# Optimization experiments

Measured on AMD Instinct MI355X. Metric: run time of the kernel, lower is better.

The kernel has to match this reference:

```python
import jax, jax.numpy as jnp
import numpy as np

INPUT_DIM = 32
HIDDEN = 64
BATCH = 4096
SEQ = 256


def _uniform(key, shape, bound):
    return jax.random.uniform(key, shape, dtype=jnp.float32, minval=-bound, maxval=bound)


def setup_inputs() -> dict:
    key = jax.random.key(0)
    ks = jax.random.split(key, 16)
    kb = 1.0 / np.sqrt(HIDDEN)  # torch LSTM/Linear init bound
    x = jax.random.normal(ks[0], (BATCH, SEQ, INPUT_DIM), dtype=jnp.float32)
    # LSTM layer 0 (input_dim -> hidden), gate order i,f,g,o stacked on dim 0
    Wih0 = _uniform(ks[1], (4 * HIDDEN, INPUT_DIM), kb)
    Whh0 = _uniform(ks[2], (4 * HIDDEN, HIDDEN), kb)
    bih0 = _uniform(ks[3], (4 * HIDDEN,), kb)
    bhh0 = _uniform(ks[4], (4 * HIDDEN,), kb)
    # LSTM layer 1 (hidden -> hidden)
    Wih1 = _uniform(ks[5], (4 * HIDDEN, HIDDEN), kb)
    Whh1 = _uniform(ks[6], (4 * HIDDEN, HIDDEN), kb)
    bih1 = _uniform(ks[7], (4 * HIDDEN,), kb)
    bhh1 = _uniform(ks[8], (4 * HIDDEN,), kb)
    # MLP head
    W1 = _uniform(ks[9], (HIDDEN, HIDDEN), kb)
    b1 = _uniform(ks[10], (HIDDEN,), kb)
    W2 = _uniform(ks[11], (1, HIDDEN), kb)
    b2 = _uniform(ks[12], (1,), kb)
    return {"x": x, "Wih0": Wih0, "Whh0": Whh0, "bih0": bih0, "bhh0": bhh0,
            "Wih1": Wih1, "Whh1": Whh1, "bih1": bih1, "bhh1": bhh1,
            "W1": W1, "b1": b1, "W2": W2, "b2": b2}


def lstm_layer(x, Wih, Whh, bih, bhh):
    """x: [B,T,D] -> hidden sequence [B,T,H]. PyTorch gate order i,f,g,o."""
    B = x.shape[0]
    H = Whh.shape[1]
    # precompute input contribution for all timesteps: [B,T,4H]
    gx = jnp.einsum('btd,gd->btg', x, Wih) + bih + bhh

    def step(carry, g_t):
        h, c = carry
        g = g_t + h @ Whh.T  # [B,4H]
        i, f, gg, o = jnp.split(g, 4, axis=-1)
        i = jax.nn.sigmoid(i)
        f = jax.nn.sigmoid(f)
        gg = jnp.tanh(gg)
        o = jax.nn.sigmoid(o)
        c = f * c + i * gg
        h = o * jnp.tanh(c)
        return (h, c), h

    h0 = jnp.zeros((B, H), x.dtype)
    c0 = jnp.zeros((B, H), x.dtype)
    _, hs = jax.lax.scan(step, (h0, c0), jnp.swapaxes(gx, 0, 1))  # hs: [T,B,H]
    return jnp.swapaxes(hs, 0, 1)


def reference(x, Wih0, Whh0, bih0, bhh0, Wih1, Whh1, bih1, bhh1, W1, b1, W2, b2):
    h1 = lstm_layer(x, Wih0, Whh0, bih0, bhh0)    # [B,T,H]
    h2 = lstm_layer(h1, Wih1, Whh1, bih1, bhh1)   # [B,T,H]
    last = h2[:, -1, :]                            # [B,H]
    f = jax.nn.relu(last @ W1.T + b1)              # dropout = identity (eval)
    out = f @ W2.T + b2                            # [B,1]
    return out
```

## Files before the change

### kernel.cpp

```cpp
#include <hip/hip_runtime.h>
#include <cstdint>

typedef __attribute__((ext_vector_type(8))) _Float16 f16x8;
typedef __attribute__((ext_vector_type(4))) float f32x4;

#define SEQL 256

#define WS_B0H   0
#define WS_B0L   49152
#define WS_B1H   98304
#define WS_BIAS0 229376
#define WS_BIAS1 230400

#define ASTR 656
#define L_A  0
#define L_HD 10496
#define HDSTR 272
#define LDS_TOTAL 14848

#define NEG_L   -1.4426950408889634f
#define NEG_2L  -2.8853900817779268f
#define LO_SCALE 2048.0f
#define LO_INV   4.8828125e-4f

__device__ __forceinline__ float ex2(float x) { return __builtin_amdgcn_exp2f(x); }
__device__ __forceinline__ float rcp_(float x) { return __builtin_amdgcn_rcpf(x); }
__device__ __forceinline__ f32x4 mfma16(f16x8 a, f16x8 b, f32x4 c) {
  return __builtin_amdgcn_mfma_f32_16x16x32_f16(a, b, c, 0, 0, 0);
}
__device__ __forceinline__ f16x8 zero8() {
  f16x8 z;
#pragma unroll
  for (int i = 0; i < 8; ++i) z[i] = (_Float16)0.f;
  return z;
}

__global__ __launch_bounds__(256) void prep(
    const float* __restrict__ Wih0, const float* __restrict__ Whh0,
    const float* __restrict__ bih0, const float* __restrict__ bhh0,
    const float* __restrict__ Wih1, const float* __restrict__ Whh1,
    const float* __restrict__ bih1, const float* __restrict__ bhh1,
    unsigned char* __restrict__ ws) {
  int e = blockIdx.x * 256 + threadIdx.x;
  if (e < 24576) {
    int j = e & 7, lane = (e >> 3) & 63, nt = (e >> 9) & 15, ks = e >> 13;
    int kdim = ks * 32 + (lane >> 4) * 8 + j;
    int col = nt * 16 + (lane & 15);
    int ko = col >> 2, g = col & 3;
    float w = (kdim < 32) ? Wih0[(g * 64 + ko) * 32 + kdim]
                          : Whh0[(g * 64 + ko) * 64 + (kdim - 32)];
    w *= (g == 2) ? NEG_2L : NEG_L;
    _Float16 hi = (_Float16)w;
    _Float16 lo = (_Float16)((w - (float)hi) * LO_SCALE);
    ((_Float16*)(ws + WS_B0H))[e] = hi;
    ((_Float16*)(ws + WS_B0L))[e] = lo;
  } else if (e < 57344) {
    int r = e - 24576;
    int j = r & 7, lane = (r >> 3) & 63, nt = (r >> 9) & 15, ks = r >> 13;
    int kdim = ks * 32 + (lane >> 4) * 8 + j;
    int col = nt * 16 + (lane & 15);
    int ko = col >> 2, g = col & 3;
    float w = (kdim < 64) ? Wih1[(g * 64 + ko) * 64 + kdim]
                          : Whh1[(g * 64 + ko) * 64 + (kdim - 64)];
    w *= (g == 2) ? NEG_2L : NEG_L;
    _Float16 hi = (_Float16)w;
    _Float16 lo = (_Float16)((w - (float)hi) * LO_SCALE);
    ((_Float16*)(ws + WS_B1H))[r] = hi;
    ((_Float16*)(ws + WS_B1H + 65536))[r] = lo;
  } else if (e < 57856) {
    int r = e - 57344;
    int col = r & 255, ko = col >> 2, g = col & 3;
    float v = (r < 256) ? bih0[g * 64 + ko] + bhh0[g * 64 + ko]
                        : bih1[g * 64 + ko] + bhh1[g * 64 + ko];
    v *= (g == 2) ? NEG_2L : NEG_L;
    ((float*)(ws + (r < 256 ? WS_BIAS0 : WS_BIAS1)))[col] = v;
  }
}

__global__ __launch_bounds__(1024, 4) void lstm_mfma8(
    const float* __restrict__ x, const unsigned char* __restrict__ ws,
    const float* __restrict__ W1, const float* __restrict__ b1,
    const float* __restrict__ W2, const float* __restrict__ b2,
    float* __restrict__ out) {
  __shared__ __align__(16) unsigned char lds[LDS_TOTAL];
  const int tid = threadIdx.x;
  const int lane = tid & 63, wave = tid >> 6;
  const int q = lane >> 4, mcol = lane & 15;
  const bool grpA = wave < 8;

  f16x8 b0h[3], b0l[3], b1h[4], b1l[4];
#pragma unroll
  for (int ks = 0; ks < 3; ++ks) {
    int rec = (ks * 16 + wave) * 64 + lane;
    b0h[ks] = ((const f16x8*)(ws + WS_B0H))[rec];
    b0l[ks] = ((const f16x8*)(ws + WS_B0L))[rec];
  }
#pragma unroll
  for (int ks = 0; ks < 4; ++ks) {
    int rec = (ks * 16 + wave) * 64 + lane;
    b1h[ks] = ((const f16x8*)(ws + WS_B1H))[rec];
    b1l[ks] = ((const f16x8*)(ws + WS_B1H + 65536))[rec];
  }
  const f32x4 bias0v = ((const f32x4*)(ws + WS_BIAS0))[wave * 4 + q];
  const f32x4 bias1v = ((const f32x4*)(ws + WS_BIAS1))[wave * 4 + q];
  f32x4 z4;
  z4[0] = z4[1] = z4[2] = z4[3] = 0.f;

  for (int i = tid; i < 2624; i += 1024) ((unsigned*)(lds + L_A))[i] = 0u;

  const bool do_x = tid < 512;
  const int bx = tid >> 5, d = tid & 31;
  const float* xcol = x + (size_t)(blockIdx.x * 16 + (do_x ? bx : 0)) * (SEQL * 32) + d;
  if (do_x) {
    *(_Float16*)(lds + L_A + bx * ASTR + d * 2) = (_Float16)xcol[0];
  }

  const int ard = mcol * ASTR + q * 16;
  const int hwr = mcol * ASTR + (wave * 4 + q) * 2;

  float c1 = 0.f, c2 = 0.f, h2f = 0.f;
  f16x8 ah1[2], ah2[2], ax;
  ah1[0] = ah1[1] = ah2[0] = ah2[1] = zero8();
  __syncthreads();
  ax = *(const f16x8*)(lds + L_A + ard + 0);

  auto cell = [&](const f32x4& aH, const f32x4& aL, float& c) -> float {
    float p0 = fmaf(aL[0], LO_INV, aH[0]);
    float p1 = fmaf(aL[1], LO_INV, aH[1]);
    float p2 = fmaf(aL[2], LO_INV, aH[2]);
    float p3 = fmaf(aL[3], LO_INV, aH[3]);
    float gi = rcp_(1.f + ex2(p0));
    float gf = rcp_(1.f + ex2(p1));
    float gg = fmaf(2.f, rcp_(1.f + ex2(p2)), -1.f);
    float go = rcp_(1.f + ex2(p3));
    c = fmaf(gf, c, gi * gg);
    float tc = fmaf(2.f, rcp_(1.f + ex2(c * NEG_2L)), -1.f);
    return go * tc;
  };

  auto iter = [&](int t, int par, bool doL2) {
    const int h1s = 128 + par * 128;
    const int h2s = 384 + par * 128;
    const int xwr = (par ^ 1) * 64;
    int tn = t + 1; if (tn > SEQL - 1) tn = SEQL - 1;
    float xnext = do_x ? xcol[tn * 32] : 0.f;

    f32x4 aH0, aL0, aH1, aL1;
    auto mG0 = [&] {
      __builtin_amdgcn_s_setprio(1);
      aH0 = mfma16(b0h[0], ax, bias0v);
      aL0 = mfma16(b0l[0], ax, z4);
      aH0 = mfma16(b0h[1], ah1[0], aH0);
      aL0 = mfma16(b0l[1], ah1[0], aL0);
      aH0 = mfma16(b0h[2], ah1[1], aH0);
      aL0 = mfma16(b0l[2], ah1[1], aL0);
      __builtin_amdgcn_s_setprio(0);
    };
    auto cG0 = [&] {
      float h1 = cell(aH0, aL0, c1);
      *(_Float16*)(lds + L_A + hwr + h1s) = (_Float16)h1;
    };
    auto mG1 = [&] {
      __builtin_amdgcn_s_setprio(1);
      aH1 = mfma16(b1h[0], ah1[0], bias1v);
      aL1 = mfma16(b1l[0], ah1[0], z4);
      aH1 = mfma16(b1h[1], ah1[1], aH1);
      aL1 = mfma16(b1l[1], ah1[1], aL1);
      aH1 = mfma16(b1h[2], ah2[0], aH1);
      aL1 = mfma16(b1l[2], ah2[0], aL1);
      aH1 = mfma16(b1h[3], ah2[1], aH1);
      aL1 = mfma16(b1l[3], ah2[1], aL1);
      __builtin_amdgcn_s_setprio(0);
    };
    auto cG1 = [&] {
      if (doL2) {
        float h2 = cell(aH1, aL1, c2);
        *(_Float16*)(lds + L_A + hwr + h2s) = (_Float16)h2;
      }
    };

    if (grpA) { mG0(); cG0(); mG1(); cG1(); }
    else      { mG1(); cG1(); mG0(); cG0(); }

    if (do_x) {
      *(_Float16*)(lds + L_A + bx * ASTR + xwr + d * 2) = (_Float16)xnext;
    }
    __syncthreads();
    ax     = *(const f16x8*)(lds + L_A + ard + xwr);
    ah1[0] = *(const f16x8*)(lds + L_A + ard + h1s);
    ah1[1] = *(const f16x8*)(lds + L_A + ard + h1s + 64);
    ah2[0] = *(const f16x8*)(lds + L_A + ard + h2s);
    ah2[1] = *(const f16x8*)(lds + L_A + ard + h2s + 64);
  };

  iter(0, 0, false);
#pragma unroll 1
  for (int tp = 0; tp < 127; ++tp) {
    iter(2 * tp + 1, 1, true);
    iter(2 * tp + 2, 0, true);
  }
  iter(255, 1, true);

  {
    f32x4 aH = mfma16(b1h[0], ah1[0], bias1v);
    f32x4 aL = mfma16(b1l[0], ah1[0], z4);
    aH = mfma16(b1h[1], ah1[1], aH);
    aL = mfma16(b1l[1], ah1[1], aL);
#pragma unroll
    for (int ks = 0; ks < 2; ++ks) {
      aH = mfma16(b1h[ks + 2], ah2[ks], aH);
      aL = mfma16(b1l[ks + 2], ah2[ks], aL);
    }
    h2f = cell(aH, aL, c2);
  }

  __syncthreads();
  *(float*)(lds + L_HD + mcol * HDSTR + (wave * 4 + q) * 4) = h2f;
  __syncthreads();
  if (tid < 256) {
    const int s = tid & 15, bo = tid >> 4;
    const float* h2row = (const float*)(lds + L_HD + bo * HDSTR);
    float partial = 0.f;
#pragma unroll
    for (int kk4 = 0; kk4 < 4; ++kk4) {
      int kk = s * 4 + kk4;
      float f = b1[kk];
#pragma unroll
      for (int j = 0; j < 64; j += 4) {
        f32x4 w = *(const f32x4*)(W1 + kk * 64 + j);
        f = fmaf(w[0], h2row[j], f);
        f = fmaf(w[1], h2row[j + 1], f);
        f = fmaf(w[2], h2row[j + 2], f);
        f = fmaf(w[3], h2row[j + 3], f);
      }
      f = fmaxf(f, 0.f);
      partial = fmaf(f, W2[kk], partial);
    }
    partial += __shfl_xor(partial, 8, 64);
    partial += __shfl_xor(partial, 4, 64);
    partial += __shfl_xor(partial, 2, 64);
    partial += __shfl_xor(partial, 1, 64);
    if (s == 0) out[blockIdx.x * 16 + bo] = partial + b2[0];
  }
}

extern "C" void kernel_launch(void* const* d_in, const int* in_sizes, int n_in,
                              void* d_out, int out_size, void* d_ws, size_t ws_size,
                              hipStream_t stream) {
  const float* x    = (const float*)d_in[0];
  const float* Wih0 = (const float*)d_in[1];
  const float* Whh0 = (const float*)d_in[2];
  const float* bih0 = (const float*)d_in[3];
  const float* bhh0 = (const float*)d_in[4];
  const float* Wih1 = (const float*)d_in[5];
  const float* Whh1 = (const float*)d_in[6];
  const float* bih1 = (const float*)d_in[7];
  const float* bhh1 = (const float*)d_in[8];
  const float* W1   = (const float*)d_in[9];
  const float* b1   = (const float*)d_in[10];
  const float* W2   = (const float*)d_in[11];
  const float* b2   = (const float*)d_in[12];
  unsigned char* ws = (unsigned char*)d_ws;
  float* out = (float*)d_out;

  prep<<<(57856 + 255) / 256, 256, 0, stream>>>(Wih0, Whh0, bih0, bhh0,
                                                Wih1, Whh1, bih1, bhh1, ws);
  lstm_mfma8<<<256, 1024, 0, stream>>>(x, ws, W1, b1, W2, b2, out);
}
```

Measured before the change: 494.5 us.

## Load x directly into MFMA registers, pack h writes, and merge gate activations

Each lane now loads its x fragment straight from global memory into registers, prefetched two steps ahead and converted to fp16. This removes the LDS staging of x and shrinks the LDS tile. The h outputs are paired across lanes with a shuffle so that half the lanes write 32-bit words, and the weights' hidden dimension is permuted to match. The cell math merges reciprocals (i*g and o*tanh(c) each use one rcp). The per-wave grouped MFMA ordering and setprio are replaced by a single interleaved MFMA sequence. The x fragment is now loaded redundantly by every wave, and the new reciprocal form needs a clamp to avoid overflow.

```diff
diff --git a/kernel.cpp b/kernel.cpp
--- a/kernel.cpp
+++ b/kernel.cpp
@@ -12,11 +12,10 @@
 #define WS_BIAS0 229376
 #define WS_BIAS1 230400
 
-#define ASTR 656
-#define L_A  0
-#define L_HD 10496
+#define ASTR 528
+#define L_HD 8448
 #define HDSTR 272
-#define LDS_TOTAL 14848
+#define LDS_TOTAL 12800
 
 #define NEG_L   -1.4426950408889634f
 #define NEG_2L  -2.8853900817779268f
@@ -33,6 +32,24 @@
 #pragma unroll
   for (int i = 0; i < 8; ++i) z[i] = (_Float16)0.f;
   return z;
+}
+__device__ __forceinline__ f16x8 cvt8(f32x4 a, f32x4 b) {
+  f16x8 r;
+#pragma unroll
+  for (int j = 0; j < 4; ++j) r[j] = (_Float16)a[j];
+#pragma unroll
+  for (int j = 0; j < 4; ++j) r[4 + j] = (_Float16)b[j];
+  return r;
+}
+__device__ __forceinline__ unsigned f16bits(float h) {
+  _Float16 hf = (_Float16)h;
+  unsigned short us;
+  __builtin_memcpy(&us, &hf, 2);
+  return (unsigned)us;
+}
+
+__device__ __forceinline__ int cp(int p) {
+  return (p & ~3) | ((p & 1) << 1) | ((p >> 1) & 1);
 }
 
 __global__ __launch_bounds__(256) void prep(
@@ -48,7 +65,7 @@
     int col = nt * 16 + (lane & 15);
     int ko = col >> 2, g = col & 3;
     float w = (kdim < 32) ? Wih0[(g * 64 + ko) * 32 + kdim]
-                          : Whh0[(g * 64 + ko) * 64 + (kdim - 32)];
+                          : Whh0[(g * 64 + ko) * 64 + cp(kdim - 32)];
     w *= (g == 2) ? NEG_2L : NEG_L;
     _Float16 hi = (_Float16)w;
     _Float16 lo = (_Float16)((w - (float)hi) * LO_SCALE);
@@ -60,8 +77,8 @@
     int kdim = ks * 32 + (lane >> 4) * 8 + j;
     int col = nt * 16 + (lane & 15);
     int ko = col >> 2, g = col & 3;
-    float w = (kdim < 64) ? Wih1[(g * 64 + ko) * 64 + kdim]
-                          : Whh1[(g * 64 + ko) * 64 + (kdim - 64)];
+    float w = (kdim < 64) ? Wih1[(g * 64 + ko) * 64 + cp(kdim)]
+                          : Whh1[(g * 64 + ko) * 64 + cp(kdim - 64)];
     w *= (g == 2) ? NEG_2L : NEG_L;
     _Float16 hi = (_Float16)w;
     _Float16 lo = (_Float16)((w - (float)hi) * LO_SCALE);
@@ -77,7 +94,7 @@
   }
 }
 
-__global__ __launch_bounds__(1024, 4) void lstm_mfma8(
+__global__ __launch_bounds__(1024, 4) void lstm_mfma12(
     const float* __restrict__ x, const unsigned char* __restrict__ ws,
     const float* __restrict__ W1, const float* __restrict__ b1,
     const float* __restrict__ W2, const float* __restrict__ b2,
@@ -86,7 +103,6 @@
   const int tid = threadIdx.x;
   const int lane = tid & 63, wave = tid >> 6;
   const int q = lane >> 4, mcol = lane & 15;
-  const bool grpA = wave < 8;
 
   f16x8 b0h[3], b0l[3], b1h[4], b1l[4];
 #pragma unroll
@@ -106,91 +122,77 @@
   f32x4 z4;
   z4[0] = z4[1] = z4[2] = z4[3] = 0.f;
 
-  for (int i = tid; i < 2624; i += 1024) ((unsigned*)(lds + L_A))[i] = 0u;
-
-  const bool do_x = tid < 512;
-  const int bx = tid >> 5, d = tid & 31;
-  const float* xcol = x + (size_t)(blockIdx.x * 16 + (do_x ? bx : 0)) * (SEQL * 32) + d;
-  if (do_x) {
-    *(_Float16*)(lds + L_A + bx * ASTR + d * 2) = (_Float16)xcol[0];
-  }
+  for (int i = tid; i < 2112; i += 1024) ((unsigned*)lds)[i] = 0u;
+
+  const float* xp = x + (size_t)(blockIdx.x * 16 + mcol) * (SEQL * 32) + q * 8;
+  f16x8 ax = cvt8(*(const f32x4*)(xp), *(const f32x4*)(xp + 4));
+  f32x4 xa = *(const f32x4*)(xp + 32);
 
   const int ard = mcol * ASTR + q * 16;
-  const int hwr = mcol * ASTR + (wave * 4 + q) * 2;
 
   float c1 = 0.f, c2 = 0.f, h2f = 0.f;
-  f16x8 ah1[2], ah2[2], ax;
+  f16x8 ah1[2], ah2[2];
   ah1[0] = ah1[1] = ah2[0] = ah2[1] = zero8();
   __syncthreads();
-  ax = *(const f16x8*)(lds + L_A + ard + 0);
 
   auto cell = [&](const f32x4& aH, const f32x4& aL, float& c) -> float {
     float p0 = fmaf(aL[0], LO_INV, aH[0]);
     float p1 = fmaf(aL[1], LO_INV, aH[1]);
     float p2 = fmaf(aL[2], LO_INV, aH[2]);
     float p3 = fmaf(aL[3], LO_INV, aH[3]);
-    float gi = rcp_(1.f + ex2(p0));
-    float gf = rcp_(1.f + ex2(p1));
-    float gg = fmaf(2.f, rcp_(1.f + ex2(p2)), -1.f);
-    float go = rcp_(1.f + ex2(p3));
-    c = fmaf(gf, c, gi * gg);
-    float tc = fmaf(2.f, rcp_(1.f + ex2(c * NEG_2L)), -1.f);
-    return go * tc;
+    float A = ex2(p0), F = ex2(p1), B = ex2(p2), C = ex2(p3);
+    float ig = (1.f - B) * rcp_((1.f + A) * (1.f + B));
+    float gf = rcp_(1.f + F);
+    c = fmaf(gf, c, ig);
+    float D = ex2(fminf(c * NEG_2L, 100.f));
+    return (1.f - D) * rcp_((1.f + C) * (1.f + D));
   };
 
+  auto hwrite = [&](float h, int slot) {
+    int hb = (int)f16bits(h);
+    int partner = __shfl_xor(hb, 32, 64);
+    if (lane < 32) {
+      unsigned v = ((unsigned)hb & 0xffffu) | ((unsigned)partner << 16);
+      *(unsigned*)(lds + mcol * ASTR + slot + wave * 8 + q * 4) = v;
+    }
+  };
+
   auto iter = [&](int t, int par, bool doL2) {
-    const int h1s = 128 + par * 128;
-    const int h2s = 384 + par * 128;
-    const int xwr = (par ^ 1) * 64;
-    int tn = t + 1; if (tn > SEQL - 1) tn = SEQL - 1;
-    float xnext = do_x ? xcol[tn * 32] : 0.f;
+    const int h1s = par * 128;
+    const int h2s = 256 + par * 128;
+    const int tn1 = (t + 1 < SEQL) ? t + 1 : SEQL - 1;
+    const int tn2 = (t + 2 < SEQL) ? t + 2 : SEQL - 1;
+    f32x4 xb = *(const f32x4*)(xp + tn1 * 32 + 4);
 
     f32x4 aH0, aL0, aH1, aL1;
-    auto mG0 = [&] {
-      __builtin_amdgcn_s_setprio(1);
-      aH0 = mfma16(b0h[0], ax, bias0v);
-      aL0 = mfma16(b0l[0], ax, z4);
-      aH0 = mfma16(b0h[1], ah1[0], aH0);
-      aL0 = mfma16(b0l[1], ah1[0], aL0);
-      aH0 = mfma16(b0h[2], ah1[1], aH0);
-      aL0 = mfma16(b0l[2], ah1[1], aL0);
-      __builtin_amdgcn_s_setprio(0);
-    };
-    auto cG0 = [&] {
-      float h1 = cell(aH0, aL0, c1);
-      *(_Float16*)(lds + L_A + hwr + h1s) = (_Float16)h1;
-    };
-    auto mG1 = [&] {
-      __builtin_amdgcn_s_setprio(1);
-      aH1 = mfma16(b1h[0], ah1[0], bias1v);
-      aL1 = mfma16(b1l[0], ah1[0], z4);
-      aH1 = mfma16(b1h[1], ah1[1], aH1);
-      aL1 = mfma16(b1l[1], ah1[1], aL1);
-      aH1 = mfma16(b1h[2], ah2[0], aH1);
-      aL1 = mfma16(b1l[2], ah2[0], aL1);
-      aH1 = mfma16(b1h[3], ah2[1], aH1);
-      aL1 = mfma16(b1l[3], ah2[1], aL1);
-      __builtin_amdgcn_s_setprio(0);
-    };
-    auto cG1 = [&] {
-      if (doL2) {
-        float h2 = cell(aH1, aL1, c2);
-        *(_Float16*)(lds + L_A + hwr + h2s) = (_Float16)h2;
-      }
-    };
-
-    if (grpA) { mG0(); cG0(); mG1(); cG1(); }
-    else      { mG1(); cG1(); mG0(); cG0(); }
-
-    if (do_x) {
-      *(_Float16*)(lds + L_A + bx * ASTR + xwr + d * 2) = (_Float16)xnext;
-    }
+    aH0 = mfma16(b0h[0], ax, bias0v);
+    aL0 = mfma16(b0l[0], ax, z4);
+    aH1 = mfma16(b1h[0], ah1[0], bias1v);
+    aL1 = mfma16(b1l[0], ah1[0], z4);
+    aH0 = mfma16(b0h[1], ah1[0], aH0);
+    aL0 = mfma16(b0l[1], ah1[0], aL0);
+    aH1 = mfma16(b1h[1], ah1[1], aH1);
+    aL1 = mfma16(b1l[1], ah1[1], aL1);
+    aH0 = mfma16(b0h[2], ah1[1], aH0);
+    aL0 = mfma16(b0l[2], ah1[1], aL0);
+    aH1 = mfma16(b1h[2], ah2[0], aH1);
+    aL1 = mfma16(b1l[2], ah2[0], aL1);
+    aH1 = mfma16(b1h[3], ah2[1], aH1);
+    aL1 = mfma16(b1l[3], ah2[1], aL1);
+
+    float h1 = cell(aH0, aL0, c1);
+    hwrite(h1, h1s);
+    if (doL2) {
+      float h2 = cell(aH1, aL1, c2);
+      hwrite(h2, h2s);
+    }
+    ax = cvt8(xa, xb);
+    xa = *(const f32x4*)(xp + tn2 * 32);
     __syncthreads();
-    ax     = *(const f16x8*)(lds + L_A + ard + xwr);
-    ah1[0] = *(const f16x8*)(lds + L_A + ard + h1s);
-    ah1[1] = *(const f16x8*)(lds + L_A + ard + h1s + 64);
-    ah2[0] = *(const f16x8*)(lds + L_A + ard + h2s);
-    ah2[1] = *(const f16x8*)(lds + L_A + ard + h2s + 64);
+    ah1[0] = *(const f16x8*)(lds + ard + h1s);
+    ah1[1] = *(const f16x8*)(lds + ard + h1s + 64);
+    ah2[0] = *(const f16x8*)(lds + ard + h2s);
+    ah2[1] = *(const f16x8*)(lds + ard + h2s + 64);
   };
 
   iter(0, 0, false);
@@ -265,5 +267,5 @@
 
   prep<<<(57856 + 255) / 256, 256, 0, stream>>>(Wih0, Whh0, bih0, bhh0,
                                                 Wih1, Whh1, bih1, bhh1, ws);
-  lstm_mfma8<<<256, 1024, 0, stream>>>(x, ws, W1, b1, W2, b2, out);
-}
+  lstm_mfma12<<<256, 1024, 0, stream>>>(x, ws, W1, b1, W2, b2, out);
+}
```

Result: faster. 455.6 us (-7.9%).
